# Kernel tuning notes

Measured on AMD Instinct MI355X. Metric: run time of the kernel, lower is better.

Reference implementation:

```python
import jax, jax.numpy as jnp
import numpy as np

D_MODEL, HEADS, GROUPS, DIM_HEAD = 256, 8, 8, 64
INNER = HEADS * DIM_HEAD              # 512
OFF_DIMS = INNER // GROUPS            # 64 channels fed to the offset network per group
DF, OFF_SCALE, KS, PAD = 4, 4.0, 6, 1  # downsample_factor, offset_scale, kernel, (6-4)//2
CPB_DIM = D_MODEL // 4                # 64
NUM_LAYERS = 6
SCALE = DIM_HEAD ** -0.5
B, H, W = 1, 40, 40


def grouped_conv1x1(x, w, g):
    # x: (b, cin, h, w); w: (cout, cin//g) torch grouped 1x1 conv weight (squeezed)
    b, cin, h, wd = x.shape
    cout = w.shape[0]
    xg = x.reshape(b, g, cin // g, h, wd)
    wg = w.reshape(g, cout // g, cin // g)
    return jnp.einsum('goi,bgihw->bgohw', wg, xg).reshape(b, cout, h, wd)


def create_grid(h, w, dtype):
    # torch meshgrid(arange(w), arange(h), indexing='xy') stacked at dim 0
    ys, xs = jnp.meshgrid(jnp.arange(h, dtype=dtype), jnp.arange(w, dtype=dtype), indexing='ij')
    return jnp.stack((xs, ys))  # (2, h, w): channel0 = x, channel1 = y


def normalize_grid(grid):
    # faithful to source: channel0 scaled by (h-1), channel1 by (w-1); out dim last
    h, w = grid.shape[-2:]
    g0 = 2.0 * grid[..., 0, :, :] / max(h - 1, 1) - 1.0
    g1 = 2.0 * grid[..., 1, :, :] / max(w - 1, 1) - 1.0
    return jnp.stack((g0, g1), axis=-1)


def grid_sample_bilinear(img, grid):
    # torch F.grid_sample, mode='bilinear', padding_mode='zeros', align_corners=False
    Bn, C, Hh, Ww = img.shape
    gx = ((grid[..., 0] + 1.0) * Ww - 1.0) * 0.5
    gy = ((grid[..., 1] + 1.0) * Hh - 1.0) * 0.5
    x0 = jnp.floor(gx)
    y0 = jnp.floor(gy)
    wx1 = gx - x0
    wy1 = gy - y0
    flat = img.reshape(Bn, C, Hh * Ww)

    def gather(xi, yi):
        valid = (xi >= 0) & (xi <= Ww - 1) & (yi >= 0) & (yi <= Hh - 1)
        xc = jnp.clip(xi, 0, Ww - 1).astype(jnp.int32)
        yc = jnp.clip(yi, 0, Hh - 1).astype(jnp.int32)
        idx = (yc * Ww + xc).reshape(Bn, 1, -1)
        vals = jnp.take_along_axis(flat, idx, axis=2).reshape(Bn, C, *xi.shape[1:])
        return vals * valid[:, None].astype(img.dtype)

    return (gather(x0, y0) * ((1 - wx1) * (1 - wy1))[:, None]
            + gather(x0 + 1, y0) * (wx1 * (1 - wy1))[:, None]
            + gather(x0, y0 + 1) * ((1 - wx1) * wy1)[:, None]
            + gather(x0 + 1, y0 + 1) * (wx1 * wy1)[:, None])


def deform_attn(x, wq, wk, wv, w_off1, b_off1, w_off2,
                cpb_w0, cpb_b0, cpb_w1, cpb_b1, cpb_w2, cpb_b2, w_out, b_out):
    b, c, Hh, Ww = x.shape
    bg = b * GROUPS
    q = grouped_conv1x1(x, wq, GROUPS)                      # (b, 512, H, W)
    qg = q.reshape(bg, OFF_DIMS, Hh, Ww)                    # group heads: (b g) d h w
    # offset network: depthwise 6x6 stride-4 conv -> GELU -> 1x1 -> tanh * scale
    off = jax.lax.conv_general_dilated(
        qg, w_off1, (DF, DF), ((PAD, PAD), (PAD, PAD)),
        dimension_numbers=('NCHW', 'OIHW', 'NCHW'), feature_group_count=OFF_DIMS)
    off = jax.nn.gelu(off + b_off1[None, :, None, None], approximate=False)
    off = jnp.tanh(jnp.einsum('oc,bchw->bohw', w_off2, off)) * OFF_SCALE  # (bg,2,h',w')
    hp, wp = off.shape[-2:]
    vgrid = create_grid(hp, wp, x.dtype)[None] + off
    vgrid_scaled = normalize_grid(vgrid)                    # (bg, h', w', 2)
    xg = x.reshape(bg, c // GROUPS, Hh, Ww)
    kv = grid_sample_bilinear(xg, vgrid_scaled).reshape(b, c, hp, wp)
    k = grouped_conv1x1(kv, wk, GROUPS)
    v = grouped_conv1x1(kv, wv, GROUPS)
    i, j = Hh * Ww, hp * wp
    qh = (q * SCALE).reshape(b, HEADS, DIM_HEAD, i).transpose(0, 1, 3, 2)  # bhid
    kh = k.reshape(b, HEADS, DIM_HEAD, j).transpose(0, 1, 3, 2)
    vh = v.reshape(b, HEADS, DIM_HEAD, j).transpose(0, 1, 3, 2)
    sim = jnp.einsum('bhid,bhjd->bhij', qh, kh)
    # continuous positional bias (CPB, depth-2 MLP on signed-log relative coords)
    grid_q = normalize_grid(create_grid(Hh, Ww, x.dtype)).reshape(i, 2)
    grid_kv = vgrid_scaled.reshape(bg, j, 2)
    pos = grid_q[None, :, None, :] - grid_kv[:, None, :, :]  # (bg, i, j, 2)
    bias = jnp.sign(pos) * jnp.log1p(jnp.abs(pos))
    bias = jax.nn.relu(bias @ cpb_w0.T + cpb_b0)
    bias = jax.nn.relu(bias @ cpb_w1.T + cpb_b1)
    bias = bias @ cpb_w2.T + cpb_b2                          # (bg, i, j, 1)
    sim = sim + bias.reshape(b, GROUPS, i, j)                # heads//offset_groups == 1
    attn = jax.nn.softmax(sim, axis=-1)                      # stable softmax (matches amax-subtract)
    out = jnp.einsum('bhij,bhjd->bhid', attn, vh)
    out = out.transpose(0, 1, 3, 2).reshape(b, INNER, Hh, Ww)
    return jnp.einsum('oc,bchw->bohw', w_out, out) + b_out[None, :, None, None]


def setup_inputs() -> dict:
    key = jax.random.key(0)
    ks = jax.random.split(key, 16)
    L = NUM_LAYERS

    def p(k, shape, scale=0.02):
        return jax.random.normal(k, shape, dtype=jnp.float32) * scale

    return {
        'bev_feat': jax.random.normal(ks[0], (B, D_MODEL, H, W), dtype=jnp.float32),
        'wq': p(ks[1], (L, INNER, D_MODEL // GROUPS)),
        'wk': p(ks[2], (L, INNER, D_MODEL // GROUPS)),
        'wv': p(ks[3], (L, INNER, D_MODEL // GROUPS)),
        'w_off1': p(ks[4], (L, OFF_DIMS, 1, KS, KS)),
        'b_off1': jnp.zeros((L, OFF_DIMS), jnp.float32),
        'w_off2': p(ks[5], (L, 2, OFF_DIMS)),
        'cpb_w0': p(ks[6], (L, CPB_DIM, 2), 0.5),
        'cpb_b0': jnp.zeros((L, CPB_DIM), jnp.float32),
        'cpb_w1': p(ks[7], (L, CPB_DIM, CPB_DIM), 0.1),
        'cpb_b1': jnp.zeros((L, CPB_DIM), jnp.float32),
        'cpb_w2': p(ks[8], (L, 1, CPB_DIM), 0.1),
        'cpb_b2': jnp.zeros((L, 1), jnp.float32),
        'w_out': p(ks[9], (L, D_MODEL, INNER)),
        'b_out': jnp.zeros((L, D_MODEL), jnp.float32),
    }


def reference(bev_feat, wq, wk, wv, w_off1, b_off1, w_off2,
              cpb_w0, cpb_b0, cpb_w1, cpb_b1, cpb_w2, cpb_b2, w_out, b_out):
    # The source encoder loop runs `output = layer(bev_feat)` on the ORIGINAL
    # input each iteration, so only the last layer's output survives. Faithful
    # math = apply layer NUM_LAYERS-1 once (dropout in eval mode -> identity).
    l = NUM_LAYERS - 1
    return deform_attn(bev_feat, wq[l], wk[l], wv[l], w_off1[l], b_off1[l], w_off2[l],
                       cpb_w0[l], cpb_b0[l], cpb_w1[l], cpb_b1[l], cpb_w2[l], cpb_b2[l],
                       w_out[l], b_out[l])
```

## Files before the change

kernel.cpp:

```cpp
#include <hip/hip_runtime.h>
#include <math.h>


#define NP 1600
#define NJ 100

typedef _Float16 f16x8 __attribute__((ext_vector_type(8)));
typedef _Float16 f16x4 __attribute__((ext_vector_type(4)));
typedef _Float16 f16x2 __attribute__((ext_vector_type(2)));
typedef float  f32x4  __attribute__((ext_vector_type(4)));
typedef float  f32x2  __attribute__((ext_vector_type(2)));

template<int CTRL>
__device__ __forceinline__ float dpp_add(float x) {
  int y = __builtin_amdgcn_update_dpp(0, __builtin_bit_cast(int, x),
                                      CTRL, 0xf, 0xf, true);
  return x + __builtin_bit_cast(float, y);
}

__global__ __launch_bounds__(256, 4) void k_off_cpb(
    const float* __restrict__ x, const float* __restrict__ wq,
    const float* __restrict__ wdw,
    const float* __restrict__ bdw, const float* __restrict__ wo2,
    const float* __restrict__ wk, const float* __restrict__ wv,
    const float* __restrict__ w0, const float* __restrict__ b0,
    const float* __restrict__ w1, const float* __restrict__ b1v,
    const float* __restrict__ cw2, const float* __restrict__ b2,
    float* __restrict__ kout, float* __restrict__ vout_t,
    _Float16* __restrict__ bias16) {
  __shared__ float psum[4][72];
  __shared__ float su_l[40];
  __shared__ float sv_l[40];
  __shared__ _Float16 a16[40][72];
  __shared__ _Float16 c16[40][72];
  int b = blockIdx.x;
  int g = b & 7;
  int j = b >> 3;
  int gj = g * 100 + j;
  int t = threadIdx.x;
  int lane = t & 63;
  int wv_id = t >> 6;
  int oy = j / 10, ox = j - (j / 10) * 10;
  int row = lane & 15;
  int kgrp = lane >> 4;

  {
    float wqreg[32];
    const float* wqr = wq + (size_t)(g * 64 + lane) * 32;
#pragma unroll
    for (int q4 = 0; q4 < 8; ++q4) {
      f32x4 a = *(const f32x4*)(wqr + q4 * 4);
#pragma unroll
      for (int e = 0; e < 4; ++e) wqreg[q4 * 4 + e] = a[e];
    }
    const float* xg = x + g * 32 * NP;
    float acc = 0.f;
#pragma unroll
    for (int tu = 0; tu < 9; ++tu) {
      int tt = wv_id * 9 + tu;
      int ky = tt / 6, kx = tt - (tt / 6) * 6;
      int iy = oy * 4 - 1 + ky;
      int ix = ox * 4 - 1 + kx;
      if (iy >= 0 && iy < 40 && ix >= 0 && ix < 40) {
        int pix = iy * 40 + ix;
        float qv = 0.f;
#pragma unroll
        for (int ci = 0; ci < 32; ++ci)
          qv = fmaf(wqreg[ci], xg[ci * NP + pix], qv);
        acc = fmaf(wdw[lane * 36 + tt], qv, acc);
      }
    }
    psum[wv_id][lane] = acc;
  }
  __syncthreads();

  if (wv_id == 0) {
    float accd = psum[0][lane] + psum[1][lane] + psum[2][lane] + psum[3][lane]
               + bdw[lane];
    float od = 0.5f * accd * (1.0f + erff(accd * 0.70710678118654752440f));
    float px = wo2[lane] * od, py = wo2[64 + lane] * od;
#pragma unroll
    for (int m = 1; m < 64; m <<= 1) {
      px += __shfl_xor(px, m);
      py += __shfl_xor(py, m);
    }
    float ax = tanhf(px) * 4.f;
    float ay = tanhf(py) * 4.f;
    float vx = (float)ox + ax;
    float vy = (float)oy + ay;
    float g0 = 2.f * vx / 9.f - 1.f;
    float g1 = 2.f * vy / 9.f - 1.f;
    if (lane < 40) {
      float qc = (float)lane * (2.f / 39.f) - 1.f;
      float u = qc - g0;
      float vv2 = qc - g1;
      su_l[lane] = copysignf(log1pf(fabsf(u)), u);
      sv_l[lane] = copysignf(log1pf(fabsf(vv2)), vv2);
    }
    float gx = ((g0 + 1.f) * 40.f - 1.f) * 0.5f;
    float gy = ((g1 + 1.f) * 40.f - 1.f) * 0.5f;
    float x0f = floorf(gx), y0f = floorf(gy);
    float wx = gx - x0f, wy = gy - y0f;
    bool mx0 = (x0f >= 0.f) && (x0f <= 39.f);
    bool mx1 = (x0f + 1.f >= 0.f) && (x0f + 1.f <= 39.f);
    bool my0 = (y0f >= 0.f) && (y0f <= 39.f);
    bool my1 = (y0f + 1.f >= 0.f) && (y0f + 1.f <= 39.f);
    int ix0 = (int)fminf(fmaxf(x0f, 0.f), 39.f);
    int ix1 = (int)fminf(fmaxf(x0f + 1.f, 0.f), 39.f);
    int iy0 = (int)fminf(fmaxf(y0f, 0.f), 39.f);
    int iy1 = (int)fminf(fmaxf(y0f + 1.f, 0.f), 39.f);
    float w00 = (1.f - wx) * (1.f - wy) * ((mx0 && my0) ? 1.f : 0.f);
    float w10 = wx * (1.f - wy) * ((mx1 && my0) ? 1.f : 0.f);
    float w01 = (1.f - wx) * wy * ((mx0 && my1) ? 1.f : 0.f);
    float w11 = wx * wy * ((mx1 && my1) ? 1.f : 0.f);
    int b00 = iy0 * 40 + ix0, b10 = iy0 * 40 + ix1;
    int b01 = iy1 * 40 + ix0, b11 = iy1 * 40 + ix1;
    float kvc = 0.f;
    if (lane < 32) {
      const float* xc = x + (g * 32 + lane) * NP;
      kvc = w00 * xc[b00] + w10 * xc[b10] + w01 * xc[b01] + w11 * xc[b11];
    }
    const float* wkr = wk + (g * 64 + lane) * 32;
    const float* wvr = wv + (g * 64 + lane) * 32;
    float wkreg[32], wvreg[32];
#pragma unroll
    for (int q4 = 0; q4 < 8; ++q4) {
      f32x4 a = *(const f32x4*)(wkr + q4 * 4);
      f32x4 bq = *(const f32x4*)(wvr + q4 * 4);
#pragma unroll
      for (int e = 0; e < 4; ++e) { wkreg[q4 * 4 + e] = a[e]; wvreg[q4 * 4 + e] = bq[e]; }
    }
    float kacc = 0.f, vacc = 0.f;
#pragma unroll
    for (int c = 0; c < 32; ++c) {
      float kvb = __shfl(kvc, c);
      kacc = fmaf(wkreg[c], kvb, kacc);
      vacc = fmaf(wvreg[c], kvb, vacc);
    }
    kout[(g * 64 + lane) * 100 + j] = kacc;
    vout_t[(size_t)gj * 64 + lane] = vacc;
  }
  __syncthreads();

  for (int idx = t; idx < 2560; idx += 256) {
    int xi = idx >> 6, kk = idx & 63;
    a16[xi][kk] = (_Float16)fmaf(w0[2 * kk], su_l[xi], b0[kk]);
    c16[xi][kk] = (_Float16)(w0[2 * kk + 1] * sv_l[xi]);
  }

  f16x8 B[4][2];
#pragma unroll
  for (int ct = 0; ct < 4; ++ct)
#pragma unroll
    for (int s = 0; s < 2; ++s)
#pragma unroll
      for (int e = 0; e < 8; ++e)
        B[ct][s][e] = (_Float16)w1[(ct * 16 + row) * 64 + s * 32 + kgrp * 8 + e];
  float b1c[4], w2c[4];
#pragma unroll
  for (int ct = 0; ct < 4; ++ct) {
    b1c[ct] = b1v[ct * 16 + row];
    w2c[ct] = cw2[ct * 16 + row];
  }
  float bb = b2[0];
  _Float16* outp = bias16 + (size_t)gj * 1600;
  __syncthreads();

  int it0 = wv_id * 25;
  int iy = wv_id * 10;
  int ix = row;
  f16x8 zero8 = {};
  for (int it = it0; it < it0 + 25; ++it) {
    f32x4 acc[4];
#pragma unroll
    for (int ct = 0; ct < 4; ++ct) {
      acc[ct][0] = 0.f; acc[ct][1] = 0.f; acc[ct][2] = 0.f; acc[ct][3] = 0.f;
    }
#pragma unroll
    for (int s = 0; s < 2; ++s) {
      f16x8 av = *(const f16x8*)&a16[ix][s * 32 + kgrp * 8];
      f16x8 cv = *(const f16x8*)&c16[iy][s * 32 + kgrp * 8];
      f16x8 A = __builtin_elementwise_max(av + cv, zero8);
#pragma unroll
      for (int ct = 0; ct < 4; ++ct)
        acc[ct] = __builtin_amdgcn_mfma_f32_16x16x32_f16(A, B[ct][s], acc[ct], 0, 0, 0);
    }
    float part[4];
#pragma unroll
    for (int ri = 0; ri < 4; ++ri) {
      float s2 = 0.f;
#pragma unroll
      for (int ct = 0; ct < 4; ++ct) {
        float val = acc[ct][ri] + b1c[ct];
        s2 = fmaf(w2c[ct], fmaxf(val, 0.f), s2);
      }
      part[ri] = s2;
    }
#pragma unroll
    for (int ri = 0; ri < 4; ++ri) {
      part[ri] = dpp_add<0xB1>(part[ri]);
      part[ri] = dpp_add<0x4E>(part[ri]);
      part[ri] = dpp_add<0x141>(part[ri]);
      part[ri] = dpp_add<0x140>(part[ri]);
    }
    if (row == 0) {
      f16x4 o;
      o[0] = (_Float16)(part[0] + bb); o[1] = (_Float16)(part[1] + bb);
      o[2] = (_Float16)(part[2] + bb); o[3] = (_Float16)(part[3] + bb);
      *(f16x4*)(outp + it * 16 + kgrp * 4) = o;
    }
    ix += 16;
    if (ix >= 40) { ix -= 40; ++iy; }
  }
}

__global__ __launch_bounds__(256) void k_attn(
    const float* __restrict__ x, const float* __restrict__ wq,
    const float* __restrict__ k, const float* __restrict__ v_t,
    const _Float16* __restrict__ bias16, float* __restrict__ inner) {
  __shared__ float v_lds[100][68];
  __shared__ float s_lds[16][100];
  __shared__ float q_lds[64][20];
  int h = blockIdx.x / 100;
  int i0 = (blockIdx.x - h * 100) * 16;
  int t = threadIdx.x;
  for (int idx = t; idx < 6400; idx += 256) {
    int j = idx >> 6, d = idx & 63;
    v_lds[j][d] = v_t[(size_t)h * 6400 + idx];
  }
  {
    int d = t & 63;
    int i4 = t >> 6;
    f32x4 wr[8];
#pragma unroll
    for (int qq = 0; qq < 8; ++qq)
      wr[qq] = *(const f32x4*)(wq + (size_t)(h * 64 + d) * 32 + qq * 4);
#pragma unroll
    for (int ii = 0; ii < 4; ++ii) {
      int i = i4 * 4 + ii;
      float acc = 0.f;
#pragma unroll
      for (int ci = 0; ci < 32; ++ci)
        acc = fmaf(wr[ci >> 2][ci & 3], x[(h * 32 + ci) * NP + i0 + i], acc);
      q_lds[d][i] = acc;
    }
  }
  __syncthreads();
  if (t < 200) {
    int ib = (t / 25) * 2, jb = (t % 25) * 4;
    const float* kp = k + h * 64 * 100 + jb;
    float a[2][4];
#pragma unroll
    for (int ii = 0; ii < 2; ++ii)
#pragma unroll
      for (int jj = 0; jj < 4; ++jj) a[ii][jj] = 0.f;
#pragma unroll 8
    for (int d = 0; d < 64; ++d) {
      f32x2 qv = *(const f32x2*)&q_lds[d][ib];
      f32x4 kv4 = *(const f32x4*)(kp + d * 100);
#pragma unroll
      for (int ii = 0; ii < 2; ++ii)
#pragma unroll
        for (int jj = 0; jj < 4; ++jj)
          a[ii][jj] = fmaf(qv[ii], kv4[jj], a[ii][jj]);
    }
    const _Float16* bcol = bias16 + (size_t)h * 100 * 1600;
#pragma unroll
    for (int jj = 0; jj < 4; ++jj) {
      f16x2 bv = *(const f16x2*)(bcol + (size_t)(jb + jj) * 1600 + i0 + ib);
#pragma unroll
      for (int ii = 0; ii < 2; ++ii)
        s_lds[ib + ii][jb + jj] = fmaf(a[ii][jj], 0.125f, (float)bv[ii]);
    }
  }
  __syncthreads();
  {
    int i = t >> 4, sub = t & 15;
    float m = -1e30f;
    for (int j = sub; j < 100; j += 16) m = fmaxf(m, s_lds[i][j]);
#pragma unroll
    for (int off = 1; off < 16; off <<= 1) m = fmaxf(m, __shfl_xor(m, off));
    float sum = 0.f;
    for (int j = sub; j < 100; j += 16) {
      float e = expf(s_lds[i][j] - m);
      s_lds[i][j] = e;
      sum += e;
    }
#pragma unroll
    for (int off = 1; off < 16; off <<= 1) sum += __shfl_xor(sum, off);
    float inv = 1.f / sum;
    for (int j = sub; j < 100; j += 16) s_lds[i][j] *= inv;
  }
  __syncthreads();
  {
    int i = t & 15, db = (t >> 4) * 4;
    float acc[4];
#pragma unroll
    for (int dd = 0; dd < 4; ++dd) acc[dd] = 0.f;
    for (int jc = 0; jc < 25; ++jc) {
      f32x4 sv = *(const f32x4*)&s_lds[i][jc * 4];
#pragma unroll
      for (int jj = 0; jj < 4; ++jj) {
        f32x4 vv = *(const f32x4*)&v_lds[jc * 4 + jj][db];
#pragma unroll
        for (int dd = 0; dd < 4; ++dd)
          acc[dd] = fmaf(sv[jj], vv[dd], acc[dd]);
      }
    }
#pragma unroll
    for (int dd = 0; dd < 4; ++dd)
      inner[(h * 64 + db + dd) * NP + i0 + i] = acc[dd];
  }
}

__global__ __launch_bounds__(256) void k_proj(
    const float* __restrict__ inner, const float* __restrict__ w,
    const float* __restrict__ bo, float* __restrict__ out) {
  int oc = blockIdx.x & 31;
  int pt = blockIdx.x >> 5;
  int t = threadIdx.x;
  int quad = __builtin_amdgcn_readfirstlane(t >> 6);
  int o0 = oc * 8 + quad * 2;
  int p = pt * 64 + (t & 63);
  const float* w0r = w + (size_t)o0 * 512;
  float a0 = 0.f, a1 = 0.f;
#pragma unroll 8
  for (int c = 0; c < 512; ++c) {
    float xv = inner[c * NP + p];
    a0 = fmaf(w0r[c], xv, a0);
    a1 = fmaf(w0r[512 + c], xv, a1);
  }
  out[(o0 + 0) * NP + p] = a0 + bo[o0 + 0];
  out[(o0 + 1) * NP + p] = a1 + bo[o0 + 1];
}

extern "C" void kernel_launch(void* const* d_in, const int* in_sizes, int n_in,
                              void* d_out, int out_size, void* d_ws, size_t ws_size,
                              hipStream_t stream) {
  int L = in_sizes[1] / (512 * 32);
  int l = L - 1;
  const float* x      = (const float*)d_in[0];
  const float* wq     = (const float*)d_in[1]  + (size_t)l * 512 * 32;
  const float* wk     = (const float*)d_in[2]  + (size_t)l * 512 * 32;
  const float* wv     = (const float*)d_in[3]  + (size_t)l * 512 * 32;
  const float* w_off1 = (const float*)d_in[4]  + (size_t)l * 64 * 36;
  const float* b_off1 = (const float*)d_in[5]  + (size_t)l * 64;
  const float* w_off2 = (const float*)d_in[6]  + (size_t)l * 2 * 64;
  const float* cpb_w0 = (const float*)d_in[7]  + (size_t)l * 64 * 2;
  const float* cpb_b0 = (const float*)d_in[8]  + (size_t)l * 64;
  const float* cpb_w1 = (const float*)d_in[9]  + (size_t)l * 64 * 64;
  const float* cpb_b1 = (const float*)d_in[10] + (size_t)l * 64;
  const float* cpb_w2 = (const float*)d_in[11] + (size_t)l * 64;
  const float* cpb_b2 = (const float*)d_in[12] + (size_t)l * 1;
  const float* w_out  = (const float*)d_in[13] + (size_t)l * 256 * 512;
  const float* b_out  = (const float*)d_in[14] + (size_t)l * 256;
  float* out = (float*)d_out;

  float* ws = (float*)d_ws;
  float*    k_ws    = ws;
  float*    vt_ws   = ws + 51200;
  _Float16* bias16  = (_Float16*)(ws + 102400);
  float*    inner   = ws + 742400;

  k_off_cpb<<<800, 256, 0, stream>>>(x, wq, w_off1, b_off1, w_off2, wk, wv,
                                     cpb_w0, cpb_b0, cpb_w1, cpb_b1, cpb_w2,
                                     cpb_b2, k_ws, vt_ws, bias16);
  k_attn<<<800, 256, 0, stream>>>(x, wq, k_ws, vt_ws, bias16, inner);
  k_proj<<<800, 256, 0, stream>>>(inner, w_out, b_out, out);
}
```

Baseline: 99.56 us.

## Transpose attention output to pixel-major and vectorize projection; stage x tile in LDS

The attention kernel now writes its output pixel-major (pixel × 512 channels) with 16-byte vector stores. The projection kernel is retiled so each thread reads contiguous float4 chunks of a pixel row and two weight rows. The attention kernel also stages the 32×16 input tile in LDS instead of re-reading global memory per thread. In the offset kernel, the conv tap loop becomes branchless with clamped, wave-uniform addresses and a zeroed tap weight. The aim is better coalescing and fewer divergent loads, at the cost of strided per-thread row reads in projection and an extra barrier.

After: 170.8 us. +71.5%, slower.

```diff
diff --git a/kernel.cpp b/kernel.cpp
--- a/kernel.cpp
+++ b/kernel.cpp
@@ -61,14 +61,17 @@
       int ky = tt / 6, kx = tt - (tt / 6) * 6;
       int iy = oy * 4 - 1 + ky;
       int ix = ox * 4 - 1 + kx;
-      if (iy >= 0 && iy < 40 && ix >= 0 && ix < 40) {
-        int pix = iy * 40 + ix;
-        float qv = 0.f;
-#pragma unroll
-        for (int ci = 0; ci < 32; ++ci)
-          qv = fmaf(wqreg[ci], xg[ci * NP + pix], qv);
-        acc = fmaf(wdw[lane * 36 + tt], qv, acc);
-      }
+      bool valid = (iy >= 0 && iy < 40 && ix >= 0 && ix < 40);
+      int iyc = min(max(iy, 0), 39);
+      int ixc = min(max(ix, 0), 39);
+      int pix = __builtin_amdgcn_readfirstlane(iyc * 40 + ixc);
+      const float* xr = xg + pix;
+      float qv = 0.f;
+#pragma unroll
+      for (int ci = 0; ci < 32; ++ci)
+        qv = fmaf(wqreg[ci], xr[(size_t)ci * NP], qv);
+      float wtap = valid ? wdw[lane * 36 + tt] : 0.f;
+      acc = fmaf(wtap, qv, acc);
     }
     psum[wv_id][lane] = acc;
   }
@@ -217,10 +220,11 @@
 __global__ __launch_bounds__(256) void k_attn(
     const float* __restrict__ x, const float* __restrict__ wq,
     const float* __restrict__ k, const float* __restrict__ v_t,
-    const _Float16* __restrict__ bias16, float* __restrict__ inner) {
+    const _Float16* __restrict__ bias16, float* __restrict__ inner_t) {
   __shared__ float v_lds[100][68];
   __shared__ float s_lds[16][100];
   __shared__ float q_lds[64][20];
+  __shared__ float x_tile[32][16];
   int h = blockIdx.x / 100;
   int i0 = (blockIdx.x - h * 100) * 16;
   int t = threadIdx.x;
@@ -228,6 +232,11 @@
     int j = idx >> 6, d = idx & 63;
     v_lds[j][d] = v_t[(size_t)h * 6400 + idx];
   }
+  for (int idx = t; idx < 512; idx += 256) {
+    int ci = idx >> 4, i = idx & 15;
+    x_tile[ci][i] = x[(h * 32 + ci) * NP + i0 + i];
+  }
+  __syncthreads();
   {
     int d = t & 63;
     int i4 = t >> 6;
@@ -241,7 +250,7 @@
       float acc = 0.f;
 #pragma unroll
       for (int ci = 0; ci < 32; ++ci)
-        acc = fmaf(wr[ci >> 2][ci & 3], x[(h * 32 + ci) * NP + i0 + i], acc);
+        acc = fmaf(wr[ci >> 2][ci & 3], x_tile[ci][i], acc);
       q_lds[d][i] = acc;
     }
   }
@@ -307,28 +316,36 @@
           acc[dd] = fmaf(sv[jj], vv[dd], acc[dd]);
       }
     }
-#pragma unroll
-    for (int dd = 0; dd < 4; ++dd)
-      inner[(h * 64 + db + dd) * NP + i0 + i] = acc[dd];
+    f32x4 o4;
+#pragma unroll
+    for (int dd = 0; dd < 4; ++dd) o4[dd] = acc[dd];
+    *(f32x4*)&inner_t[(size_t)(i0 + i) * 512 + h * 64 + db] = o4;
   }
 }
 
 __global__ __launch_bounds__(256) void k_proj(
-    const float* __restrict__ inner, const float* __restrict__ w,
+    const float* __restrict__ inner_t, const float* __restrict__ w,
     const float* __restrict__ bo, float* __restrict__ out) {
-  int oc = blockIdx.x & 31;
-  int pt = blockIdx.x >> 5;
+  int b = blockIdx.x;
+  int occ = b & 7;
+  int pt = b >> 3;
   int t = threadIdx.x;
-  int quad = __builtin_amdgcn_readfirstlane(t >> 6);
-  int o0 = oc * 8 + quad * 2;
-  int p = pt * 64 + (t & 63);
-  const float* w0r = w + (size_t)o0 * 512;
+  int p = pt * 16 + (t & 15);
+  int o0 = occ * 32 + (t >> 4) * 2;
+  const float* ip = inner_t + (size_t)p * 512;
+  const float* wa = w + (size_t)o0 * 512;
+  const float* wb = w + (size_t)(o0 + 1) * 512;
   float a0 = 0.f, a1 = 0.f;
-#pragma unroll 8
-  for (int c = 0; c < 512; ++c) {
-    float xv = inner[c * NP + p];
-    a0 = fmaf(w0r[c], xv, a0);
-    a1 = fmaf(w0r[512 + c], xv, a1);
+#pragma unroll 4
+  for (int c4 = 0; c4 < 128; ++c4) {
+    f32x4 iv = *(const f32x4*)(ip + c4 * 4);
+    f32x4 w0v = *(const f32x4*)(wa + c4 * 4);
+    f32x4 w1v = *(const f32x4*)(wb + c4 * 4);
+#pragma unroll
+    for (int e = 0; e < 4; ++e) {
+      a0 = fmaf(w0v[e], iv[e], a0);
+      a1 = fmaf(w1v[e], iv[e], a1);
+    }
   }
   out[(o0 + 0) * NP + p] = a0 + bo[o0 + 0];
   out[(o0 + 1) * NP + p] = a1 + bo[o0 + 1];
@@ -360,11 +377,11 @@
   float*    k_ws    = ws;
   float*    vt_ws   = ws + 51200;
   _Float16* bias16  = (_Float16*)(ws + 102400);
-  float*    inner   = ws + 742400;
+  float*    inner_t = ws + 742400;
 
   k_off_cpb<<<800, 256, 0, stream>>>(x, wq, w_off1, b_off1, w_off2, wk, wv,
                                      cpb_w0, cpb_b0, cpb_w1, cpb_b1, cpb_w2,
                                      cpb_b2, k_ws, vt_ws, bias16);
-  k_attn<<<800, 256, 0, stream>>>(x, wq, k_ws, vt_ws, bias16, inner);
-  k_proj<<<800, 256, 0, stream>>>(inner, w_out, b_out, out);
-}
+  k_attn<<<800, 256, 0, stream>>>(x, wq, k_ws, vt_ws, bias16, inner_t);
+  k_proj<<<800, 256, 0, stream>>>(inner_t, w_out, b_out, out);
+}
```
